# Performance work log

Hardware: AMD Instinct MI355X
Metric: run time of the kernel (lower is better)

The kernel has to match this reference:

```python
import jax, jax.numpy as jnp
import numpy as np

SIG = [1, 1, 1, 1, -1]  # Cl(4,1)
NVEC = 5
GA = 1 << NVEC  # 32


def _build_gp_table():
    # Cayley table for the geometric product on blades indexed by bitmask.
    G = np.zeros((GA, GA, GA), np.float32)
    for a in range(GA):
        for b in range(GA):
            s = 0
            t = a >> 1
            while t:
                s += bin(t & b).count('1')
                t >>= 1
            sign = -1.0 if (s & 1) else 1.0
            common = a & b
            for i in range(NVEC):
                if (common >> i) & 1:
                    sign *= SIG[i]
            G[a, b, a ^ b] = sign
    return G

GP_TABLE = jnp.asarray(_build_gp_table())


def geometric_product(x, y):
    return jnp.einsum('...i,...j,ijk->...k', x, y, GP_TABLE)


def manifold_norm(x):
    # normalize each multivector onto the unit sphere in R^32
    return x / (jnp.linalg.norm(x, axis=-1, keepdims=True) + 1e-6)


def versor_linear(x, W, b):
    # channel mixing shared across multivector components: x [..., in, ga]
    return jnp.einsum('...ig,oi->...og', x, W) + b


def layer_norm2d(x, w, b):
    # LayerNorm over last two dims [D, ga] jointly
    mu = jnp.mean(x, axis=(-2, -1), keepdims=True)
    var = jnp.var(x, axis=(-2, -1), keepdims=True)
    return (x - mu) / jnp.sqrt(var + 1e-5) * w + b


def attention(x, Wq, bq, Wk, bk, Wv, bv, Wo, bo, n_heads):
    B, S, D, G = x.shape
    dh = D // n_heads
    q = versor_linear(x, Wq, bq).reshape(B, S, n_heads, dh, G)
    k = versor_linear(x, Wk, bk).reshape(B, S, n_heads, dh, G)
    v = versor_linear(x, Wv, bv).reshape(B, S, n_heads, dh, G)
    scale = 1.0 / np.sqrt(dh * G).astype(np.float32)
    scores = jnp.einsum('bshdg,bthdg->bhst', q, k) * scale
    probs = jax.nn.softmax(scores, axis=-1)
    o = jnp.einsum('bhst,bthdg->bshdg', probs, v).reshape(B, S, D, G)
    return versor_linear(o, Wo, bo)


N_HEADS = 8


def forward(x, Wq, bq, Wk, bk, Wv, bv, Wo, bo, ln1_w, ln1_b, ln2_w, ln2_b,
            gamma1, gamma2, W1, b1, W2, b2, Wr, br, Wc, bc):
    L = Wq.shape[0]
    for l in range(L):
        h = attention(layer_norm2d(x, ln1_w[l], ln1_b[l]),
                      Wq[l], bq[l], Wk[l], bk[l], Wv[l], bv[l], Wo[l], bo[l], N_HEADS)
        x = manifold_norm(x + gamma1[l] * h)
        m = versor_linear(layer_norm2d(x, ln2_w[l], ln2_b[l]), W1[l], b1[l])
        m = versor_linear(jnp.tanh(m), W2[l], b2[l])
        x = manifold_norm(x + gamma2[l] * m)
    # RecursiveRotorAccumulator: log(S)-step inclusive scan of rotors
    delta = versor_linear(x, Wr, br)
    rot = 0.5 * delta
    rot = rot.at[..., 0].add(1.0)
    rot = manifold_norm(rot)
    S = x.shape[1]
    step = 1
    while step < S:
        left = rot[:, :-step]
        right = rot[:, step:]
        comb = manifold_norm(geometric_product(right, left))
        rot = jnp.concatenate([rot[:, :step], comb], axis=1)
        step *= 2
    pooled = rot[:, -1]  # [B, D, ga]
    logits = pooled.reshape(pooled.shape[0], -1) @ Wc.T + bc
    return logits


def setup_inputs() -> dict:
    key = jax.random.key(0)
    B, S, D, G, L, NC = 8, 256, 64, GA, 4, 1000
    E = 4 * D  # expansion hidden
    ks = jax.random.split(key, 16)
    sd = 0.02
    inp = {
        'x': jax.random.normal(ks[0], (B, S, D, G), jnp.float32),
        'Wq': jax.random.normal(ks[1], (L, D, D), jnp.float32) * sd,
        'bq': jnp.zeros((L, D, G), jnp.float32),
        'Wk': jax.random.normal(ks[2], (L, D, D), jnp.float32) * sd,
        'bk': jnp.zeros((L, D, G), jnp.float32),
        'Wv': jax.random.normal(ks[3], (L, D, D), jnp.float32) * sd,
        'bv': jnp.zeros((L, D, G), jnp.float32),
        'Wo': jax.random.normal(ks[4], (L, D, D), jnp.float32) * sd,
        'bo': jnp.zeros((L, D, G), jnp.float32),
        'ln1_w': jnp.ones((L, D, G), jnp.float32),
        'ln1_b': jnp.zeros((L, D, G), jnp.float32),
        'ln2_w': jnp.ones((L, D, G), jnp.float32),
        'ln2_b': jnp.zeros((L, D, G), jnp.float32),
        'gamma1': 1e-5 * jnp.ones((L, D, G), jnp.float32),
        'gamma2': 1e-5 * jnp.ones((L, D, G), jnp.float32),
        'W1': jax.random.normal(ks[5], (L, E, D), jnp.float32) * sd,
        'b1': jnp.zeros((L, E, G), jnp.float32),
        'W2': jax.random.normal(ks[6], (L, D, E), jnp.float32) * sd,
        'b2': jnp.zeros((L, D, G), jnp.float32),
        'Wr': jax.random.normal(ks[7], (D, D), jnp.float32) * sd,
        'br': jnp.zeros((D, G), jnp.float32),
        'Wc': jax.random.normal(ks[8], (NC, D * G), jnp.float32) * sd,
        'bc': jnp.zeros((NC,), jnp.float32),
    }
    return inp


def reference(x, Wq, bq, Wk, bk, Wv, bv, Wo, bo, ln1_w, ln1_b, ln2_w, ln2_b,
              gamma1, gamma2, W1, b1, W2, b2, Wr, br, Wc, bc):
    return forward(x, Wq, bq, Wk, bk, Wv, bv, Wo, bo, ln1_w, ln1_b, ln2_w, ln2_b,
                   gamma1, gamma2, W1, b1, W2, b2, Wr, br, Wc, bc)
```

## Files before the change

kernel.cpp:

```cpp
#include <hip/hip_runtime.h>
#include <hip/hip_bf16.h>

constexpr int kB  = 8;
constexpr int kS  = 256;
constexpr int kD  = 64;
constexpr int kG  = 32;
constexpr int kE  = 256;
constexpr int kNH = 8;
constexpr int kHD = 256;
constexpr int kDG = kD * kG;
constexpr int kT  = kB * kS;
constexpr int kNC = 1000;

using bf16x8 = __attribute__((ext_vector_type(8))) short;
using f32x4  = __attribute__((ext_vector_type(4))) float;

__device__ __forceinline__ short f2bf(float f) {
    unsigned u = __float_as_uint(f);
    unsigned r = (u + 0x7FFFu + ((u >> 16) & 1u)) >> 16;
    return (short)r;
}

__device__ __forceinline__ float tanh_fast(float x) {
    float a = fabsf(x);
    float e = __expf(-2.f * a);
    float d = 1.f + e;
    float r = __builtin_amdgcn_rcpf(d);
    r = r * (2.f - d * r);
    float t = (1.f - e) * r;
    return copysignf(t, x);
}

__global__ __launch_bounds__(256) void cvtw_kernel(
    const float* __restrict__ Wq, const float* __restrict__ Wk,
    const float* __restrict__ Wv, const float* __restrict__ Wo,
    const float* __restrict__ W1, const float* __restrict__ W2,
    unsigned short* __restrict__ dst) {
    int idx = (blockIdx.x * 256 + threadIdx.x) * 4;
    const float* src; int off;
    if      (idx <  16384) { src = Wq; off = 0; }
    else if (idx <  32768) { src = Wk; off = 16384; }
    else if (idx <  49152) { src = Wv; off = 32768; }
    else if (idx <  65536) { src = Wo; off = 49152; }
    else if (idx < 131072) { src = W1; off = 65536; }
    else                   { src = W2; off = 131072; }
    const float4 v = *(const float4*)(src + (idx - off));
    *(short4*)&dst[idx] = make_short4(f2bf(v.x), f2bf(v.y), f2bf(v.z), f2bf(v.w));
}

__global__ __launch_bounds__(256) void prep_tr_kernel(
    const float* __restrict__ bq, const float* __restrict__ bk,
    const float* __restrict__ bv, const float* __restrict__ bo,
    const float* __restrict__ b2, const float* __restrict__ gm1,
    const float* __restrict__ gm2, const float* __restrict__ ln2w,
    const float* __restrict__ ln2b, const float* __restrict__ ln1w,
    const float* __restrict__ ln1b, const float* __restrict__ b1,
    float* __restrict__ dst) {
    __shared__ float lt[32 * 257];
    const int a = blockIdx.x >> 2, l = blockIdx.x & 3;
    const float* srcs[12] = {bq, bk, bv, bo, b2, gm1, gm2, ln2w, ln2b, ln1w, ln1b, b1};
    const int R  = (a == 11) ? 256 : 64;
    const int sh = (a == 11) ? 8 : 6;
    const float* src = srcs[a] + (size_t)l * R * 32;
    float* out = dst + a * 8192 + l * R * 32;
    const int tid = threadIdx.x;
    for (int j = tid; j < R * 32; j += 256) lt[(j & 31) * (R + 1) + (j >> 5)] = src[j];
    __syncthreads();
    for (int k = tid; k < R * 32; k += 256) {
        int g = k >> sh, r = k & (R - 1);
        out[k] = lt[g * (R + 1) + r];
    }
}

__global__ __launch_bounds__(256) void ln_kernel(const float* __restrict__ Xin,
                                                 const float* __restrict__ w,
                                                 const float* __restrict__ b,
                                                 unsigned short* __restrict__ A,
                                                 float* __restrict__ XT) {
    int t = blockIdx.x, tid = threadIdx.x;
    const float* xp = Xin + (size_t)t * kDG;
    __shared__ float r1[256], r2[256];
    __shared__ short st[32 * 72];
    __shared__ float xf[32 * 68];
    float v[8], s = 0.f, ss = 0.f;
#pragma unroll
    for (int j = 0; j < 8; j++) {
        float x = xp[tid + j * 256];
        v[j] = x; s += x; ss += x * x;
        int jj = tid + j * 256;
        xf[(jj & 31) * 68 + (jj >> 5)] = x;
    }
    r1[tid] = s; r2[tid] = ss; __syncthreads();
    for (int o = 128; o > 0; o >>= 1) {
        if (tid < o) { r1[tid] += r1[tid + o]; r2[tid] += r2[tid + o]; }
        __syncthreads();
    }
    float mean = r1[0] * (1.f / kDG);
    float var  = r2[0] * (1.f / kDG) - mean * mean;
    float rstd = rsqrtf(var + 1e-5f);
#pragma unroll
    for (int j = 0; j < 8; j++) {
        int jj = tid + j * 256;
        float val = (v[j] - mean) * rstd * w[jj] + b[jj];
        st[(jj & 31) * 72 + (jj >> 5)] = f2bf(val);
    }
    __syncthreads();
    bf16x8 ov = *(const bf16x8*)&st[(tid >> 3) * 72 + (tid & 7) * 8];
    *(bf16x8*)&A[(size_t)t * kDG + tid * 8] = ov;
    const int row = tid >> 3, col = (tid & 7) * 8;
    float* xo = XT + (size_t)t * kDG + tid * 8;
    *(float4*)(xo + 0) = *(const float4*)&xf[row * 68 + col + 0];
    *(float4*)(xo + 4) = *(const float4*)&xf[row * 68 + col + 4];
}

__global__ __launch_bounds__(256) void vlinT_kernel(const float* __restrict__ XT,
                                                    const float* __restrict__ W,
                                                    const float* __restrict__ bias,
                                                    float* __restrict__ OutT) {
    __shared__ float sx[32 * 65];
    __shared__ float sw[kD * kD];
    int t = blockIdx.x, tid = threadIdx.x;
    const float* xp = XT + (size_t)t * kDG;
    for (int j = tid; j < kDG; j += 256) sx[(j >> 6) * 65 + (j & 63)] = xp[j];
    for (int j = tid; j < kD * kD; j += 256) sw[j] = W[j];
    __syncthreads();
    int g = tid & 31, ob = tid >> 5;
    int b = t >> 8, s = t & 255;
    float* op = OutT + ((size_t)b * kD * kS + s) * kG;
    for (int o = ob; o < kD; o += 8) {
        float acc = bias[o * kG + g];
        const float* wr = sw + o * kD;
#pragma unroll
        for (int i = 0; i < kD; i++) acc += wr[i] * sx[g * 65 + i];
        op[(size_t)o * kS * kG + g] = acc;
    }
}

template<bool LAST>
__global__ __launch_bounds__(128, 4) void mega_kernel(
    const unsigned short* __restrict__ O,
    const unsigned short* __restrict__ Woh, const float* __restrict__ boT,
    const float* __restrict__ gm1T,
    const float* __restrict__ ln2wT, const float* __restrict__ ln2bT,
    const unsigned short* __restrict__ W1h, const float* __restrict__ b1T,
    const unsigned short* __restrict__ W2h, const float* __restrict__ b2T,
    const float* __restrict__ gm2T,
    const float* __restrict__ ln1wT, const float* __restrict__ ln1bT,
    float* __restrict__ XT,
    const unsigned short* __restrict__ Wqh, const unsigned short* __restrict__ Wkh,
    const unsigned short* __restrict__ Wvh,
    const float* __restrict__ bqT, const float* __restrict__ bkT,
    const float* __restrict__ bvT,
    unsigned short* __restrict__ Q, unsigned short* __restrict__ K,
    unsigned short* __restrict__ V) {
    constexpr int AS = 72;
    constexpr int MS = 264;
    __shared__ short sA[32 * AS];
    __shared__ short sM[32 * MS];
    __shared__ float sred[4];

    const int tid = threadIdx.x;
    const int w = tid >> 6, lane = tid & 63;
    const int l16 = lane & 15, quad = lane >> 4;
    const int tok = blockIdx.x;
    const size_t tb = (size_t)tok * kDG;

    float xv[2][2][4];
    {
        const unsigned short* xp = O + tb;
        bf16x8 bfr[2][2];
#pragma unroll
        for (int c = 0; c < 2; ++c)
#pragma unroll
            for (int nt = 0; nt < 2; ++nt)
                bfr[c][nt] = *(const bf16x8*)&xp[(nt * 16 + l16) * kD + c * 32 + quad * 8];

        f32x4 accW[2][2];
#pragma unroll
        for (int mt = 0; mt < 2; ++mt)
#pragma unroll
            for (int nt = 0; nt < 2; ++nt) accW[mt][nt] = (f32x4){0.f, 0.f, 0.f, 0.f};
#pragma unroll
        for (int mt = 0; mt < 2; ++mt)
#pragma unroll
            for (int c = 0; c < 2; ++c) {
                bf16x8 afr = *(const bf16x8*)&Woh[(w * 32 + mt * 16 + l16) * kD + c * 32 + quad * 8];
#pragma unroll
                for (int nt = 0; nt < 2; ++nt)
                    accW[mt][nt] = __builtin_amdgcn_mfma_f32_16x16x32_bf16(afr, bfr[c][nt], accW[mt][nt], 0, 0, 0);
            }

        float s = 0.f, ss = 0.f;
#pragma unroll
        for (int mt = 0; mt < 2; ++mt) {
            int o0 = w * 32 + mt * 16 + quad * 4;
            float vv[2][4];
#pragma unroll
            for (int nt = 0; nt < 2; ++nt) {
                int g = nt * 16 + l16;
                const float4 b4 = *(const float4*)&boT[g * kD + o0];
                const float4 g4 = *(const float4*)&gm1T[g * kD + o0];
                const float4 xi = *(const float4*)&XT[tb + g * kD + o0];
#pragma unroll
                for (int r = 0; r < 4; ++r)
                    vv[nt][r] = (&xi.x)[r] + (&g4.x)[r] * (accW[mt][nt][r] + (&b4.x)[r]);
            }
#pragma unroll
            for (int r = 0; r < 4; ++r) {
                float sq = vv[0][r] * vv[0][r] + vv[1][r] * vv[1][r];
#pragma unroll
                for (int off = 1; off < 16; off <<= 1) sq += __shfl_xor(sq, off, 64);
                float rn = 1.f / (sqrtf(sq) + 1e-6f);
#pragma unroll
                for (int nt = 0; nt < 2; ++nt) {
                    float x = vv[nt][r] * rn;
                    xv[mt][nt][r] = x;
                    s += x; ss = fmaf(x, x, ss);
                }
            }
        }
#pragma unroll
        for (int off = 1; off < 64; off <<= 1) {
            s += __shfl_xor(s, off, 64); ss += __shfl_xor(ss, off, 64);
        }
        if (lane == 0) { sred[w] = s; sred[2 + w] = ss; }
        __syncthreads();
        float st = sred[0] + sred[1], sst = sred[2] + sred[3];
        float mean = st * (1.f / kDG);
        float var  = sst * (1.f / kDG) - mean * mean;
        float rstd = rsqrtf(var + 1e-5f);
#pragma unroll
        for (int mt = 0; mt < 2; ++mt)
#pragma unroll
            for (int nt = 0; nt < 2; ++nt) {
                int g = nt * 16 + l16;
                int o0 = w * 32 + mt * 16 + quad * 4;
                const float4 w4 = *(const float4*)&ln2wT[g * kD + o0];
                const float4 b4 = *(const float4*)&ln2bT[g * kD + o0];
                short4 s4;
#pragma unroll
                for (int r = 0; r < 4; ++r)
                    (&s4.x)[r] = f2bf((xv[mt][nt][r] - mean) * rstd * (&w4.x)[r] + (&b4.x)[r]);
                *(short4*)&sA[g * AS + o0] = s4;
            }
    }
    __syncthreads();

    {
        bf16x8 afrA[2][2];
#pragma unroll
        for (int c = 0; c < 2; ++c)
#pragma unroll
            for (int nt = 0; nt < 2; ++nt)
                afrA[c][nt] = *(const bf16x8*)&sA[(nt * 16 + l16) * AS + c * 32 + quad * 8];

        f32x4 acc1[8][2];
#pragma unroll
        for (int mt = 0; mt < 8; ++mt)
#pragma unroll
            for (int nt = 0; nt < 2; ++nt) acc1[mt][nt] = (f32x4){0.f, 0.f, 0.f, 0.f};
#pragma unroll
        for (int mt = 0; mt < 8; ++mt)
#pragma unroll
            for (int c = 0; c < 2; ++c) {
                bf16x8 afr = *(const bf16x8*)&W1h[((w * 8 + mt) * 16 + l16) * kD + c * 32 + quad * 8];
#pragma unroll
                for (int nt = 0; nt < 2; ++nt)
                    acc1[mt][nt] = __builtin_amdgcn_mfma_f32_16x16x32_bf16(afr, afrA[c][nt], acc1[mt][nt], 0, 0, 0);
            }
#pragma unroll
        for (int mt = 0; mt < 8; ++mt)
#pragma unroll
            for (int nt = 0; nt < 2; ++nt) {
                int g = nt * 16 + l16;
                int e0 = (w * 8 + mt) * 16 + quad * 4;
                const float4 b4 = *(const float4*)&b1T[g * kE + e0];
                short4 s4;
#pragma unroll
                for (int r = 0; r < 4; ++r)
                    (&s4.x)[r] = f2bf(tanh_fast(acc1[mt][nt][r] + (&b4.x)[r]));
                *(short4*)&sM[g * MS + e0] = s4;
            }
    }
    __syncthreads();

    f32x4 acc2[2][2];
#pragma unroll
    for (int mt = 0; mt < 2; ++mt)
#pragma unroll
        for (int nt = 0; nt < 2; ++nt) acc2[mt][nt] = (f32x4){0.f, 0.f, 0.f, 0.f};
#pragma unroll
    for (int c = 0; c < 8; ++c) {
        bf16x8 bq[2];
#pragma unroll
        for (int nt = 0; nt < 2; ++nt)
            bq[nt] = *(const bf16x8*)&sM[(nt * 16 + l16) * MS + c * 32 + quad * 8];
#pragma unroll
        for (int mt = 0; mt < 2; ++mt) {
            bf16x8 afr = *(const bf16x8*)&W2h[(w * 32 + mt * 16 + l16) * kE + c * 32 + quad * 8];
#pragma unroll
            for (int nt = 0; nt < 2; ++nt)
                acc2[mt][nt] = __builtin_amdgcn_mfma_f32_16x16x32_bf16(afr, bq[nt], acc2[mt][nt], 0, 0, 0);
        }
    }

    float yv[2][2][4];
    float s2 = 0.f, ss2 = 0.f;
#pragma unroll
    for (int mt = 0; mt < 2; ++mt) {
        int o0 = w * 32 + mt * 16 + quad * 4;
        float vv[2][4];
#pragma unroll
        for (int nt = 0; nt < 2; ++nt) {
            int g = nt * 16 + l16;
            const float4 b4 = *(const float4*)&b2T[g * kD + o0];
            const float4 g4 = *(const float4*)&gm2T[g * kD + o0];
#pragma unroll
            for (int r = 0; r < 4; ++r)
                vv[nt][r] = xv[mt][nt][r] + (&g4.x)[r] * (acc2[mt][nt][r] + (&b4.x)[r]);
        }
#pragma unroll
        for (int r = 0; r < 4; ++r) {
            float sq = vv[0][r] * vv[0][r] + vv[1][r] * vv[1][r];
#pragma unroll
            for (int off = 1; off < 16; off <<= 1) sq += __shfl_xor(sq, off, 64);
            float rn = 1.f / (sqrtf(sq) + 1e-6f);
#pragma unroll
            for (int nt = 0; nt < 2; ++nt) {
                float x = vv[nt][r] * rn;
                yv[mt][nt][r] = x;
                s2 += x; ss2 = fmaf(x, x, ss2);
            }
        }
#pragma unroll
        for (int nt = 0; nt < 2; ++nt) {
            int g = nt * 16 + l16;
            float4 xo;
#pragma unroll
            for (int r = 0; r < 4; ++r) (&xo.x)[r] = yv[mt][nt][r];
            *(float4*)&XT[tb + g * kD + o0] = xo;
        }
    }
    if constexpr (LAST) return;

#pragma unroll
    for (int off = 1; off < 64; off <<= 1) {
        s2 += __shfl_xor(s2, off, 64); ss2 += __shfl_xor(ss2, off, 64);
    }
    if (lane == 0) { sred[w] = s2; sred[2 + w] = ss2; }
    __syncthreads();
    {
        float st = sred[0] + sred[1], sst = sred[2] + sred[3];
        float mean = st * (1.f / kDG);
        float var  = sst * (1.f / kDG) - mean * mean;
        float rstd = rsqrtf(var + 1e-5f);
#pragma unroll
        for (int mt = 0; mt < 2; ++mt)
#pragma unroll
            for (int nt = 0; nt < 2; ++nt) {
                int g = nt * 16 + l16;
                int o0 = w * 32 + mt * 16 + quad * 4;
                const float4 w4 = *(const float4*)&ln1wT[g * kD + o0];
                const float4 b4 = *(const float4*)&ln1bT[g * kD + o0];
                short4 s4;
#pragma unroll
                for (int r = 0; r < 4; ++r)
                    (&s4.x)[r] = f2bf((yv[mt][nt][r] - mean) * rstd * (&w4.x)[r] + (&b4.x)[r]);
                *(short4*)&sA[g * AS + o0] = s4;
            }
    }
    __syncthreads();

    {
        bf16x8 afrA[2][2];
#pragma unroll
        for (int c = 0; c < 2; ++c)
#pragma unroll
            for (int nt = 0; nt < 2; ++nt)
                afrA[c][nt] = *(const bf16x8*)&sA[(nt * 16 + l16) * AS + c * 32 + quad * 8];

        const unsigned short* Wp[3] = {Wqh, Wkh, Wvh};
        const float* Bp[3] = {bqT, bkT, bvT};
        unsigned short* Op[3] = {Q, K, V};
#pragma unroll
        for (int m = 0; m < 3; ++m) {
            f32x4 acc3[2][2];
#pragma unroll
            for (int mt = 0; mt < 2; ++mt)
#pragma unroll
                for (int nt = 0; nt < 2; ++nt) acc3[mt][nt] = (f32x4){0.f, 0.f, 0.f, 0.f};
#pragma unroll
            for (int mt = 0; mt < 2; ++mt)
#pragma unroll
                for (int c = 0; c < 2; ++c) {
                    bf16x8 afr = *(const bf16x8*)&Wp[m][(w * 32 + mt * 16 + l16) * kD + c * 32 + quad * 8];
#pragma unroll
                    for (int nt = 0; nt < 2; ++nt)
                        acc3[mt][nt] = __builtin_amdgcn_mfma_f32_16x16x32_bf16(afr, afrA[c][nt], acc3[mt][nt], 0, 0, 0);
                }
            unsigned short* op = Op[m] + tb;
#pragma unroll
            for (int mt = 0; mt < 2; ++mt)
#pragma unroll
                for (int nt = 0; nt < 2; ++nt) {
                    int g = nt * 16 + l16;
                    int o0 = w * 32 + mt * 16 + quad * 4;
                    const float4 b4 = *(const float4*)&Bp[m][g * kD + o0];
#pragma unroll
                    for (int r = 0; r < 4; ++r)
                        op[(o0 + r) * kG + g] = (unsigned short)f2bf(acc3[mt][nt][r] + (&b4.x)[r]);
                }
        }
    }
}

__global__ __launch_bounds__(256, 3) void gemm_qkv_kernel(
    const unsigned short* __restrict__ X,
    const unsigned short* __restrict__ Wqh, const unsigned short* __restrict__ Wkh,
    const unsigned short* __restrict__ Wvh,
    const float* __restrict__ bqT, const float* __restrict__ bkT, const float* __restrict__ bvT,
    unsigned short* __restrict__ Q, unsigned short* __restrict__ K, unsigned short* __restrict__ V) {
    constexpr int WS = 64 + 8;
    __shared__ short sW[3 * 64 * WS];

    const int tid = threadIdx.x, wave = tid >> 6, lane = tid & 63;
    const int l16 = lane & 15, quad = lane >> 4;
    const int tok = blockIdx.x * 4 + wave;

    const unsigned short* Wp[3] = {Wqh, Wkh, Wvh};
#pragma unroll
    for (int w = 0; w < 3; ++w)
        for (int j = tid * 8; j < 64 * 64; j += 2048) {
            int o = j >> 6, i = j & 63;
            *(bf16x8*)&sW[w * 64 * WS + o * WS + i] = *(const bf16x8*)(Wp[w] + j);
        }

    const unsigned short* xp = X + (size_t)tok * kDG;
    bf16x8 bfr[2][2];
#pragma unroll
    for (int c = 0; c < 2; ++c)
#pragma unroll
        for (int nt = 0; nt < 2; ++nt)
            bfr[c][nt] = *(const bf16x8*)&xp[(nt * 16 + l16) * kD + c * 32 + quad * 8];
    __syncthreads();

    f32x4 acc[3][4][2];
#pragma unroll
    for (int w = 0; w < 3; ++w)
#pragma unroll
        for (int mt = 0; mt < 4; ++mt)
#pragma unroll
            for (int nt = 0; nt < 2; ++nt) acc[w][mt][nt] = (f32x4){0.f, 0.f, 0.f, 0.f};

#pragma unroll
    for (int w = 0; w < 3; ++w)
#pragma unroll
        for (int mt = 0; mt < 4; ++mt)
#pragma unroll
            for (int c = 0; c < 2; ++c) {
                bf16x8 afr = *(const bf16x8*)&sW[w * 64 * WS + (mt * 16 + l16) * WS + c * 32 + quad * 8];
#pragma unroll
                for (int nt = 0; nt < 2; ++nt)
                    acc[w][mt][nt] = __builtin_amdgcn_mfma_f32_16x16x32_bf16(afr, bfr[c][nt], acc[w][mt][nt], 0, 0, 0);
            }

    unsigned short* Op[3] = {Q, K, V};
    const float* Bp[3] = {bqT, bkT, bvT};
#pragma unroll
    for (int w = 0; w < 3; ++w) {
        unsigned short* op = Op[w] + (size_t)tok * kDG;
#pragma unroll
        for (int mt = 0; mt < 4; ++mt)
#pragma unroll
            for (int nt = 0; nt < 2; ++nt) {
                int g = nt * 16 + l16;
                int o0 = mt * 16 + quad * 4;
                const float4 b4 = *(const float4*)&Bp[w][g * kD + o0];
#pragma unroll
                for (int r = 0; r < 4; ++r)
                    op[(o0 + r) * kG + g] = (unsigned short)f2bf(acc[w][mt][nt][r] + (&b4.x)[r]);
            }
    }
}

constexpr int QSTR = 264;
constexpr int VSTR = 40;

__global__ __launch_bounds__(256) void attn_mfma_kernel(const unsigned short* __restrict__ Q,
                                                        const unsigned short* __restrict__ K,
                                                        const unsigned short* __restrict__ V,
                                                        unsigned short* __restrict__ O) {
    __shared__ short sQ[64 * QSTR];
    __shared__ short sKV[2][256 * VSTR];

    const int qt = blockIdx.x, h = blockIdx.y, b = blockIdx.z;
    const int tid = threadIdx.x;
    const int wave = tid >> 6, lane = tid & 63;
    const int l16 = lane & 15, quad = lane >> 4;

    const size_t bh = (size_t)b * kS * kDG + (size_t)h * kHD;

#pragma unroll
    for (int it = 0; it < 8; ++it) {
        int j = it * 2048 + tid * 8;
        int row = j >> 8, col = j & 255;
        *(bf16x8*)&sQ[row * QSTR + col] =
            *(const bf16x8*)(Q + bh + (size_t)(qt * 64 + row) * kDG + col);
    }
#pragma unroll
    for (int it = 0; it < 4; ++it) {
        int j = it * 2048 + tid * 8;
        int row = j >> 8, col = j & 255;
        *(bf16x8*)&sKV[0][row * QSTR + col] =
            *(const bf16x8*)(K + bh + (size_t)row * kDG + col);
    }
    __syncthreads();

    bf16x8 afrag[8];
    {
        int row = wave * 16 + l16;
#pragma unroll
        for (int c = 0; c < 8; ++c)
            afrag[c] = *(const bf16x8*)&sQ[row * QSTR + c * 32 + quad * 8];
    }

    f32x4 acc[16];
#pragma unroll
    for (int i = 0; i < 16; ++i) acc[i] = (f32x4){0.f, 0.f, 0.f, 0.f};

    for (int kt = 0; kt < 8; ++kt) {
        bf16x8 kpre[4];
        if (kt < 7) {
#pragma unroll
            for (int it = 0; it < 4; ++it) {
                int j = it * 2048 + tid * 8;
                int row = j >> 8, col = j & 255;
                kpre[it] = *(const bf16x8*)(K + bh + (size_t)((kt + 1) * 32 + row) * kDG + col);
            }
        }
        const short* kb = sKV[kt & 1];
#pragma unroll
        for (int nt = 0; nt < 2; ++nt) {
            int key = nt * 16 + l16;
            f32x4 a = acc[kt * 2 + nt];
#pragma unroll
            for (int c = 0; c < 8; ++c) {
                bf16x8 bfrag = *(const bf16x8*)&kb[key * QSTR + c * 32 + quad * 8];
                a = __builtin_amdgcn_mfma_f32_16x16x32_bf16(afrag[c], bfrag, a, 0, 0, 0);
            }
            acc[kt * 2 + nt] = a;
        }
        if (kt < 7) {
            short* nb = sKV[(kt + 1) & 1];
#pragma unroll
            for (int it = 0; it < 4; ++it) {
                int j = it * 2048 + tid * 8;
                int row = j >> 8, col = j & 255;
                *(bf16x8*)&nb[row * QSTR + col] = kpre[it];
            }
            __syncthreads();
        }
    }

    float inv[4];
#pragma unroll
    for (int r = 0; r < 4; ++r) {
        float m = -1e30f;
#pragma unroll
        for (int t = 0; t < 16; ++t) m = fmaxf(m, acc[t][r]);
#pragma unroll
        for (int off = 1; off < 16; off <<= 1) m = fmaxf(m, __shfl_xor(m, off, 16));
        float s = 0.f;
#pragma unroll
        for (int t = 0; t < 16; ++t) {
            float p = __expf((acc[t][r] - m) * 0.0625f);
            acc[t][r] = p; s += p;
        }
#pragma unroll
        for (int off = 1; off < 16; off <<= 1) s += __shfl_xor(s, off, 16);
        inv[r] = 1.f / s;
    }

#pragma unroll
    for (int t = 0; t < 16; ++t)
#pragma unroll
        for (int r = 0; r < 4; ++r)
            sQ[(wave * 16 + quad * 4 + r) * QSTR + t * 16 + l16] = f2bf(acc[t][r]);

    {
        int kb = tid >> 5;
#pragma unroll
        for (int it = 0; it < 2; ++it) {
            int db = (tid & 31) + it * 32;
            short4 vr[4];
#pragma unroll
            for (int r = 0; r < 4; ++r)
                vr[r] = *(const short4*)(V + bh + (size_t)(kb * 4 + r) * kDG + db * 4);
#pragma unroll
            for (int i = 0; i < 4; ++i) {
                short4 p = make_short4((&vr[0].x)[i], (&vr[1].x)[i],
                                       (&vr[2].x)[i], (&vr[3].x)[i]);
                *(short4*)&sKV[0][(db * 4 + i) * VSTR + kb * 4] = p;
            }
        }
    }
    __syncthreads();

    f32x4 oacc[16];
#pragma unroll
    for (int i = 0; i < 16; ++i) oacc[i] = (f32x4){0.f, 0.f, 0.f, 0.f};

    for (int vt = 0; vt < 8; ++vt) {
        short4 vpre[8];
        if (vt < 7) {
            int kb = tid >> 5;
#pragma unroll
            for (int it = 0; it < 2; ++it) {
                int db = (tid & 31) + it * 32;
#pragma unroll
                for (int r = 0; r < 4; ++r)
                    vpre[it * 4 + r] = *(const short4*)(V + bh + (size_t)((vt + 1) * 32 + kb * 4 + r) * kDG + db * 4);
            }
        }
        const short* vb = sKV[vt & 1];
        bf16x8 pfrag = *(const bf16x8*)&sQ[(wave * 16 + l16) * QSTR + vt * 32 + quad * 8];
#pragma unroll
        for (int dt = 0; dt < 16; ++dt) {
            bf16x8 vfrag = *(const bf16x8*)&vb[(dt * 16 + l16) * VSTR + quad * 8];
            oacc[dt] = __builtin_amdgcn_mfma_f32_16x16x32_bf16(pfrag, vfrag, oacc[dt], 0, 0, 0);
        }
        if (vt < 7) {
            short* nb = sKV[(vt + 1) & 1];
            int kb = tid >> 5;
#pragma unroll
            for (int it = 0; it < 2; ++it) {
                int db = (tid & 31) + it * 32;
#pragma unroll
                for (int i = 0; i < 4; ++i) {
                    short4 p = make_short4((&vpre[it * 4 + 0].x)[i], (&vpre[it * 4 + 1].x)[i],
                                           (&vpre[it * 4 + 2].x)[i], (&vpre[it * 4 + 3].x)[i]);
                    *(short4*)&nb[(db * 4 + i) * VSTR + kb * 4] = p;
                }
            }
            __syncthreads();
        }
    }

    {
        const size_t ob = (size_t)(b * kS + qt * 64 + wave * 16 + quad * 4) * kDG + h * 8;
#pragma unroll
        for (int gg = 0; gg < 2; ++gg) {
            int g = gg * 16 + l16;
#pragma unroll
            for (int r = 0; r < 4; ++r) {
                bf16x8 pk;
#pragma unroll
                for (int k = 0; k < 8; ++k)
                    pk[k] = f2bf(oacc[k * 2 + gg][r] * inv[r]);
                *(bf16x8*)&O[ob + (size_t)r * kDG + g * kD] = pk;
            }
        }
    }
}

constexpr int pc_ce(unsigned v) { int c = 0; while (v) { c += v & 1; v >>= 1; } return c; }
constexpr unsigned gp_mask_ce(int a) {
    unsigned m = 0;
    for (int c = 0; c < 32; ++c) {
        int b = a ^ c;
        int s = (a & b) >> 4;
        for (int t = a >> 1; t; t >>= 1) s += pc_ce(t & b);
        if (s & 1) m |= (1u << c);
    }
    return m;
}

template<int A>
__device__ __forceinline__ void gp_term(const float* x, const float* y, float* acc) {
    constexpr unsigned m = gp_mask_ce(A);
    const float xa = x[A], nxa = -xa;
#pragma unroll
    for (int c = 0; c < 32; ++c)
        acc[c] = fmaf(((m >> c) & 1u) ? nxa : xa, y[A ^ c], acc[c]);
}

__device__ __forceinline__ void gp_mn_t(const float* x, const float* y, float* out) {
    float acc[32];
#pragma unroll
    for (int c = 0; c < 32; ++c) acc[c] = 0.f;
    gp_term<0>(x, y, acc);  gp_term<1>(x, y, acc);  gp_term<2>(x, y, acc);  gp_term<3>(x, y, acc);
    gp_term<4>(x, y, acc);  gp_term<5>(x, y, acc);  gp_term<6>(x, y, acc);  gp_term<7>(x, y, acc);
    gp_term<8>(x, y, acc);  gp_term<9>(x, y, acc);  gp_term<10>(x, y, acc); gp_term<11>(x, y, acc);
    gp_term<12>(x, y, acc); gp_term<13>(x, y, acc); gp_term<14>(x, y, acc); gp_term<15>(x, y, acc);
    gp_term<16>(x, y, acc); gp_term<17>(x, y, acc); gp_term<18>(x, y, acc); gp_term<19>(x, y, acc);
    gp_term<20>(x, y, acc); gp_term<21>(x, y, acc); gp_term<22>(x, y, acc); gp_term<23>(x, y, acc);
    gp_term<24>(x, y, acc); gp_term<25>(x, y, acc); gp_term<26>(x, y, acc); gp_term<27>(x, y, acc);
    gp_term<28>(x, y, acc); gp_term<29>(x, y, acc); gp_term<30>(x, y, acc); gp_term<31>(x, y, acc);
    float ss = 0.f;
#pragma unroll
    for (int c = 0; c < 32; ++c) ss = fmaf(acc[c], acc[c], ss);
    float r = 1.f / (sqrtf(ss) + 1e-6f);
#pragma unroll
    for (int c = 0; c < 32; ++c) out[c] = acc[c] * r;
}

__device__ __forceinline__ void leaf_load(const float* base, float* v) {
#pragma unroll
    for (int i = 0; i < 8; ++i) {
        const float4 f = *(const float4*)(base + i * 4);
        v[i * 4 + 0] = 0.5f * f.x; v[i * 4 + 1] = 0.5f * f.y;
        v[i * 4 + 2] = 0.5f * f.z; v[i * 4 + 3] = 0.5f * f.w;
    }
    v[0] += 1.f;
    float ss = 0.f;
#pragma unroll
    for (int c = 0; c < 32; ++c) ss = fmaf(v[c], v[c], ss);
    float r = 1.f / (sqrtf(ss) + 1e-6f);
#pragma unroll
    for (int c = 0; c < 32; ++c) v[c] *= r;
}

__global__ __launch_bounds__(256) void scanreg_kernel(const float* __restrict__ DT,
                                                      float* __restrict__ pooled) {
    const int wave = threadIdx.x >> 6, lane = threadIdx.x & 63;
    const int seq = blockIdx.x * 4 + wave;
    const float* base = DT + ((size_t)seq * kS + lane * 4) * kG;

    float R[32], Y[32], P[32], Xa[32], Yb[32];

    leaf_load(base, R);
    for (int j = 1; j < 4; ++j) {
        leaf_load(base + j * kG, Y);
        gp_mn_t(Y, R, R);
    }

    for (int step = 1; step < 64; step <<= 1) {
        const bool up = lane & step;
#pragma unroll
        for (int c = 0; c < 32; ++c) P[c] = __shfl_xor(R[c], step, 64);
#pragma unroll
        for (int c = 0; c < 32; ++c) {
            Xa[c] = up ? R[c] : P[c];
            Yb[c] = up ? P[c] : R[c];
        }
        gp_mn_t(Xa, Yb, R);
    }

    if (lane == 0) {
        float* op = pooled + (size_t)seq * kG;
#pragma unroll
        for (int i = 0; i < 8; ++i)
            *(float4*)(op + i * 4) = make_float4(R[i * 4], R[i * 4 + 1], R[i * 4 + 2], R[i * 4 + 3]);
    }
}

__global__ __launch_bounds__(256) void cls2_kernel(const float* __restrict__ P,
                                                   const float* __restrict__ Wc,
                                                   const float* __restrict__ bc,
                                                   float* __restrict__ out) {
    __shared__ float sp[kB * kDG];
    const int tid = threadIdx.x, wave = tid >> 6, lane = tid & 63;
    for (int j = tid * 4; j < kB * kDG; j += 1024)
        *(float4*)&sp[j] = *(const float4*)(P + j);
    __syncthreads();

    const int c = blockIdx.x * 4 + wave;
    const float* w = Wc + (size_t)c * kDG;
    float acc[kB];
#pragma unroll
    for (int b = 0; b < kB; ++b) acc[b] = 0.f;
#pragma unroll
    for (int cc = 0; cc < 8; ++cc) {
        const float4 w4 = *(const float4*)(w + cc * 256 + lane * 4);
#pragma unroll
        for (int b = 0; b < kB; ++b) {
            const float4 p4 = *(const float4*)&sp[b * kDG + cc * 256 + lane * 4];
            acc[b] += w4.x * p4.x + w4.y * p4.y + w4.z * p4.z + w4.w * p4.w;
        }
    }
#pragma unroll
    for (int b = 0; b < kB; ++b)
#pragma unroll
        for (int off = 32; off > 0; off >>= 1) acc[b] += __shfl_xor(acc[b], off, 64);
    if (lane == 0) {
        float bias = bc[c];
#pragma unroll
        for (int b = 0; b < kB; ++b) out[b * kNC + c] = acc[b] + bias;
    }
}

extern "C" void kernel_launch(void* const* d_in, const int* in_sizes, int n_in,
                              void* d_out, int out_size, void* d_ws, size_t ws_size,
                              hipStream_t stream) {
    const float* x_in = (const float*)d_in[0];
    const float* Wq   = (const float*)d_in[1];
    const float* bq   = (const float*)d_in[2];
    const float* Wk   = (const float*)d_in[3];
    const float* bk   = (const float*)d_in[4];
    const float* Wv   = (const float*)d_in[5];
    const float* bv   = (const float*)d_in[6];
    const float* Wo   = (const float*)d_in[7];
    const float* bo   = (const float*)d_in[8];
    const float* ln1w = (const float*)d_in[9];
    const float* ln1b = (const float*)d_in[10];
    const float* ln2w = (const float*)d_in[11];
    const float* ln2b = (const float*)d_in[12];
    const float* gm1  = (const float*)d_in[13];
    const float* gm2  = (const float*)d_in[14];
    const float* W1   = (const float*)d_in[15];
    const float* b1   = (const float*)d_in[16];
    const float* W2   = (const float*)d_in[17];
    const float* b2   = (const float*)d_in[18];
    const float* Wr   = (const float*)d_in[19];
    const float* br   = (const float*)d_in[20];
    const float* Wc   = (const float*)d_in[21];
    const float* bc   = (const float*)d_in[22];

    const size_t NEL = (size_t)kT * kDG;
    float* F  = (float*)d_ws;
    float* XT = F;
    unsigned short* Abf = (unsigned short*)(F + NEL);
    unsigned short* Qh = (unsigned short*)(F + 2 * NEL);
    unsigned short* Kh = (unsigned short*)(F + 3 * NEL);
    unsigned short* Vh = (unsigned short*)(F + 4 * NEL);
    unsigned short* Wb = (unsigned short*)(F + 5 * NEL);
    float* PT = F + 3 * NEL + NEL / 2;
    float* pooled = F + 2 * NEL;
    float* DT = F + NEL;

    cvtw_kernel<<<192, 256, 0, stream>>>(Wq, Wk, Wv, Wo, W1, W2, Wb);
    prep_tr_kernel<<<48, 256, 0, stream>>>(bq, bk, bv, bo, b2, gm1, gm2,
                                           ln2w, ln2b, ln1w, ln1b, b1, PT);
    unsigned short* Wqh = Wb;
    unsigned short* Wkh = Wb + 16384;
    unsigned short* Wvh = Wb + 32768;
    unsigned short* Woh = Wb + 49152;
    unsigned short* W1h = Wb + 65536;
    unsigned short* W2h = Wb + 131072;

    auto bqT   = [&](int l) { return PT + 0     + l * 2048; };
    auto bkT   = [&](int l) { return PT + 8192  + l * 2048; };
    auto bvT   = [&](int l) { return PT + 16384 + l * 2048; };
    auto boT   = [&](int l) { return PT + 24576 + l * 2048; };
    auto b2T   = [&](int l) { return PT + 32768 + l * 2048; };
    auto gm1T  = [&](int l) { return PT + 40960 + l * 2048; };
    auto gm2T  = [&](int l) { return PT + 49152 + l * 2048; };
    auto ln2wT = [&](int l) { return PT + 57344 + l * 2048; };
    auto ln2bT = [&](int l) { return PT + 65536 + l * 2048; };
    auto ln1wT = [&](int l) { return PT + 73728 + l * 2048; };
    auto ln1bT = [&](int l) { return PT + 81920 + l * 2048; };
    auto b1T   = [&](int l) { return PT + 90112 + l * 8192; };

    ln_kernel<<<kT, 256, 0, stream>>>(x_in, ln1w, ln1b, Abf, XT);
    gemm_qkv_kernel<<<kT / 4, 256, 0, stream>>>(Abf,
        Wqh, Wkh, Wvh, bqT(0), bkT(0), bvT(0), Qh, Kh, Vh);

    for (int l = 0; l < 4; l++) {
        attn_mfma_kernel<<<dim3(4, kNH, kB), 256, 0, stream>>>(Qh, Kh, Vh, Abf);
        if (l < 3)
            mega_kernel<false><<<kT, 128, 0, stream>>>(Abf,
                Woh + l * 4096, boT(l), gm1T(l), ln2wT(l), ln2bT(l),
                W1h + l * 16384, b1T(l), W2h + l * 16384, b2T(l), gm2T(l),
                ln1wT(l + 1), ln1bT(l + 1), XT,
                Wqh + (l + 1) * 4096, Wkh + (l + 1) * 4096, Wvh + (l + 1) * 4096,
                bqT(l + 1), bkT(l + 1), bvT(l + 1), Qh, Kh, Vh);
        else
            mega_kernel<true><<<kT, 128, 0, stream>>>(Abf,
                Woh + l * 4096, boT(l), gm1T(l), ln2wT(l), ln2bT(l),
                W1h + l * 16384, b1T(l), W2h + l * 16384, b2T(l), gm2T(l),
                nullptr, nullptr, XT,
                nullptr, nullptr, nullptr, nullptr, nullptr, nullptr,
                nullptr, nullptr, nullptr);
    }

    vlinT_kernel<<<kT, 256, 0, stream>>>(XT, Wr, br, DT);
    scanreg_kernel<<<kB * kD / 4, 256, 0, stream>>>(DT, pooled);
    cls2_kernel<<<kNC / 4, 256, 0, stream>>>(pooled, Wc, bc, (float*)d_out);
}
```

Measured before the change: 521.1 us.

## Prefetch MLP/QKV weight fragments early and halve attention query tile

```diff
diff --git a/kernel.cpp b/kernel.cpp
--- a/kernel.cpp
+++ b/kernel.cpp
@@ -137,7 +137,7 @@
 }
 
 template<bool LAST>
-__global__ __launch_bounds__(128, 4) void mega_kernel(
+__global__ __launch_bounds__(128, 3) void mega_kernel(
     const unsigned short* __restrict__ O,
     const unsigned short* __restrict__ Woh, const float* __restrict__ boT,
     const float* __restrict__ gm1T,
@@ -166,6 +166,7 @@
     const size_t tb = (size_t)tok * kDG;
 
     float xv[2][2][4];
+    bf16x8 w1f[8];
     {
         const unsigned short* xp = O + tb;
         bf16x8 bfr[2][2];
@@ -189,6 +190,12 @@
                 for (int nt = 0; nt < 2; ++nt)
                     accW[mt][nt] = __builtin_amdgcn_mfma_f32_16x16x32_bf16(afr, bfr[c][nt], accW[mt][nt], 0, 0, 0);
             }
+
+#pragma unroll
+        for (int mt = 0; mt < 4; ++mt)
+#pragma unroll
+            for (int c = 0; c < 2; ++c)
+                w1f[mt * 2 + c] = *(const bf16x8*)&W1h[((w * 8 + mt) * 16 + l16) * kD + c * 32 + quad * 8];
 
         float s = 0.f, ss = 0.f;
 #pragma unroll
@@ -246,6 +253,7 @@
     }
     __syncthreads();
 
+    bf16x8 w2f[16];
     {
         bf16x8 afrA[2][2];
 #pragma unroll
@@ -254,22 +262,28 @@
             for (int nt = 0; nt < 2; ++nt)
                 afrA[c][nt] = *(const bf16x8*)&sA[(nt * 16 + l16) * AS + c * 32 + quad * 8];
 
-        f32x4 acc1[8][2];
-#pragma unroll
-        for (int mt = 0; mt < 8; ++mt)
+        f32x4 acc1[4][2];
+#pragma unroll
+        for (int mt = 0; mt < 4; ++mt)
 #pragma unroll
             for (int nt = 0; nt < 2; ++nt) acc1[mt][nt] = (f32x4){0.f, 0.f, 0.f, 0.f};
 #pragma unroll
-        for (int mt = 0; mt < 8; ++mt)
-#pragma unroll
-            for (int c = 0; c < 2; ++c) {
-                bf16x8 afr = *(const bf16x8*)&W1h[((w * 8 + mt) * 16 + l16) * kD + c * 32 + quad * 8];
+        for (int mt = 0; mt < 4; ++mt)
+#pragma unroll
+            for (int c = 0; c < 2; ++c)
 #pragma unroll
                 for (int nt = 0; nt < 2; ++nt)
-                    acc1[mt][nt] = __builtin_amdgcn_mfma_f32_16x16x32_bf16(afr, afrA[c][nt], acc1[mt][nt], 0, 0, 0);
-            }
-#pragma unroll
-        for (int mt = 0; mt < 8; ++mt)
+                    acc1[mt][nt] = __builtin_amdgcn_mfma_f32_16x16x32_bf16(w1f[mt * 2 + c], afrA[c][nt], acc1[mt][nt], 0, 0, 0);
+
+        bf16x8 w1g[8];
+#pragma unroll
+        for (int mt = 0; mt < 4; ++mt)
+#pragma unroll
+            for (int c = 0; c < 2; ++c)
+                w1g[mt * 2 + c] = *(const bf16x8*)&W1h[((w * 8 + 4 + mt) * 16 + l16) * kD + c * 32 + quad * 8];
+
+#pragma unroll
+        for (int mt = 0; mt < 4; ++mt)
 #pragma unroll
             for (int nt = 0; nt < 2; ++nt) {
                 int g = nt * 16 + l16;
@@ -281,6 +295,39 @@
                     (&s4.x)[r] = f2bf(tanh_fast(acc1[mt][nt][r] + (&b4.x)[r]));
                 *(short4*)&sM[g * MS + e0] = s4;
             }
+
+        f32x4 acc1b[4][2];
+#pragma unroll
+        for (int mt = 0; mt < 4; ++mt)
+#pragma unroll
+            for (int nt = 0; nt < 2; ++nt) acc1b[mt][nt] = (f32x4){0.f, 0.f, 0.f, 0.f};
+#pragma unroll
+        for (int mt = 0; mt < 4; ++mt)
+#pragma unroll
+            for (int c = 0; c < 2; ++c)
+#pragma unroll
+                for (int nt = 0; nt < 2; ++nt)
+                    acc1b[mt][nt] = __builtin_amdgcn_mfma_f32_16x16x32_bf16(w1g[mt * 2 + c], afrA[c][nt], acc1b[mt][nt], 0, 0, 0);
+
+#pragma unroll
+        for (int mt = 0; mt < 2; ++mt)
+#pragma unroll
+            for (int c = 0; c < 8; ++c)
+                w2f[mt * 8 + c] = *(const bf16x8*)&W2h[(w * 32 + mt * 16 + l16) * kE + c * 32 + quad * 8];
+
+#pragma unroll
+        for (int mt = 0; mt < 4; ++mt)
+#pragma unroll
+            for (int nt = 0; nt < 2; ++nt) {
+                int g = nt * 16 + l16;
+                int e0 = (w * 8 + 4 + mt) * 16 + quad * 4;
+                const float4 b4 = *(const float4*)&b1T[g * kE + e0];
+                short4 s4;
+#pragma unroll
+                for (int r = 0; r < 4; ++r)
+                    (&s4.x)[r] = f2bf(tanh_fast(acc1b[mt][nt][r] + (&b4.x)[r]));
+                *(short4*)&sM[g * MS + e0] = s4;
+            }
     }
     __syncthreads();
 
@@ -296,12 +343,22 @@
         for (int nt = 0; nt < 2; ++nt)
             bq[nt] = *(const bf16x8*)&sM[(nt * 16 + l16) * MS + c * 32 + quad * 8];
 #pragma unroll
-        for (int mt = 0; mt < 2; ++mt) {
-            bf16x8 afr = *(const bf16x8*)&W2h[(w * 32 + mt * 16 + l16) * kE + c * 32 + quad * 8];
+        for (int mt = 0; mt < 2; ++mt)
 #pragma unroll
             for (int nt = 0; nt < 2; ++nt)
-                acc2[mt][nt] = __builtin_amdgcn_mfma_f32_16x16x32_bf16(afr, bq[nt], acc2[mt][nt], 0, 0, 0);
-        }
+                acc2[mt][nt] = __builtin_amdgcn_mfma_f32_16x16x32_bf16(w2f[mt * 8 + c], bq[nt], acc2[mt][nt], 0, 0, 0);
+    }
+
+    bf16x8 wqf[12];
+    if constexpr (!LAST) {
+        const unsigned short* Wp[3] = {Wqh, Wkh, Wvh};
+#pragma unroll
+        for (int m = 0; m < 3; ++m)
+#pragma unroll
+            for (int mt = 0; mt < 2; ++mt)
+#pragma unroll
+                for (int c = 0; c < 2; ++c)
+                    wqf[m * 4 + mt * 2 + c] = *(const bf16x8*)&Wp[m][(w * 32 + mt * 16 + l16) * kD + c * 32 + quad * 8];
     }
 
     float yv[2][2][4];
@@ -379,7 +436,6 @@
             for (int nt = 0; nt < 2; ++nt)
                 afrA[c][nt] = *(const bf16x8*)&sA[(nt * 16 + l16) * AS + c * 32 + quad * 8];
 
-        const unsigned short* Wp[3] = {Wqh, Wkh, Wvh};
         const float* Bp[3] = {bqT, bkT, bvT};
         unsigned short* Op[3] = {Q, K, V};
 #pragma unroll
@@ -392,12 +448,10 @@
 #pragma unroll
             for (int mt = 0; mt < 2; ++mt)
 #pragma unroll
-                for (int c = 0; c < 2; ++c) {
-                    bf16x8 afr = *(const bf16x8*)&Wp[m][(w * 32 + mt * 16 + l16) * kD + c * 32 + quad * 8];
+                for (int c = 0; c < 2; ++c)
 #pragma unroll
                     for (int nt = 0; nt < 2; ++nt)
-                        acc3[mt][nt] = __builtin_amdgcn_mfma_f32_16x16x32_bf16(afr, afrA[c][nt], acc3[mt][nt], 0, 0, 0);
-                }
+                        acc3[mt][nt] = __builtin_amdgcn_mfma_f32_16x16x32_bf16(wqf[m * 4 + mt * 2 + c], afrA[c][nt], acc3[mt][nt], 0, 0, 0);
             unsigned short* op = Op[m] + tb;
 #pragma unroll
             for (int mt = 0; mt < 2; ++mt)
@@ -486,11 +540,11 @@
 constexpr int QSTR = 264;
 constexpr int VSTR = 40;
 
-__global__ __launch_bounds__(256) void attn_mfma_kernel(const unsigned short* __restrict__ Q,
+__global__ __launch_bounds__(128) void attn_mfma_kernel(const unsigned short* __restrict__ Q,
                                                         const unsigned short* __restrict__ K,
                                                         const unsigned short* __restrict__ V,
                                                         unsigned short* __restrict__ O) {
-    __shared__ short sQ[64 * QSTR];
+    __shared__ short sQ[32 * QSTR];
     __shared__ short sKV[2][256 * VSTR];
 
     const int qt = blockIdx.x, h = blockIdx.y, b = blockIdx.z;
@@ -502,14 +556,14 @@
 
 #pragma unroll
     for (int it = 0; it < 8; ++it) {
-        int j = it * 2048 + tid * 8;
+        int j = it * 1024 + tid * 8;
         int row = j >> 8, col = j & 255;
         *(bf16x8*)&sQ[row * QSTR + col] =
-            *(const bf16x8*)(Q + bh + (size_t)(qt * 64 + row) * kDG + col);
-    }
-#pragma unroll
-    for (int it = 0; it < 4; ++it) {
-        int j = it * 2048 + tid * 8;
+            *(const bf16x8*)(Q + bh + (size_t)(qt * 32 + row) * kDG + col);
+    }
+#pragma unroll
+    for (int it = 0; it < 8; ++it) {
+        int j = it * 1024 + tid * 8;
         int row = j >> 8, col = j & 255;
         *(bf16x8*)&sKV[0][row * QSTR + col] =
             *(const bf16x8*)(K + bh + (size_t)row * kDG + col);
@@ -529,11 +583,11 @@
     for (int i = 0; i < 16; ++i) acc[i] = (f32x4){0.f, 0.f, 0.f, 0.f};
 
     for (int kt = 0; kt < 8; ++kt) {
-        bf16x8 kpre[4];
+        bf16x8 kpre[8];
         if (kt < 7) {
 #pragma unroll
-            for (int it = 0; it < 4; ++it) {
-                int j = it * 2048 + tid * 8;
+            for (int it = 0; it < 8; ++it) {
+                int j = it * 1024 + tid * 8;
                 int row = j >> 8, col = j & 255;
                 kpre[it] = *(const bf16x8*)(K + bh + (size_t)((kt + 1) * 32 + row) * kDG + col);
             }
@@ -553,8 +607,8 @@
         if (kt < 7) {
             short* nb = sKV[(kt + 1) & 1];
 #pragma unroll
-            for (int it = 0; it < 4; ++it) {
-                int j = it * 2048 + tid * 8;
+            for (int it = 0; it < 8; ++it) {
+                int j = it * 1024 + tid * 8;
                 int row = j >> 8, col = j & 255;
                 *(bf16x8*)&nb[row * QSTR + col] = kpre[it];
             }
@@ -588,21 +642,19 @@
             sQ[(wave * 16 + quad * 4 + r) * QSTR + t * 16 + l16] = f2bf(acc[t][r]);
 
     {
-        int kb = tid >> 5;
-#pragma unroll
-        for (int it = 0; it < 2; ++it) {
-            int db = (tid & 31) + it * 32;
-            short4 vr[4];
-#pragma unroll
-            for (int r = 0; r < 4; ++r)
-                vr[r] = *(const short4*)(V + bh + (size_t)(kb * 4 + r) * kDG + db * 4);
-#pragma unroll
-            for (int i = 0; i < 4; ++i) {
-                short4 p = make_short4((&vr[0].x)[i], (&vr[1].x)[i],
-                                       (&vr[2].x)[i], (&vr[3].x)[i]);
-                *(short4*)&sKV[0][(db * 4 + i) * VSTR + kb * 4] = p;
-            }
-        }
+        const int db = tid & 63, kh = tid >> 6;
+        short4 vr[16];
+#pragma unroll
+        for (int r = 0; r < 16; ++r)
+            vr[r] = *(const short4*)(V + bh + (size_t)(kh * 16 + r) * kDG + db * 4);
+#pragma unroll
+        for (int i = 0; i < 4; ++i)
+#pragma unroll
+            for (int gq = 0; gq < 4; ++gq) {
+                short4 p = make_short4((&vr[gq * 4 + 0].x)[i], (&vr[gq * 4 + 1].x)[i],
+                                       (&vr[gq * 4 + 2].x)[i], (&vr[gq * 4 + 3].x)[i]);
+                *(short4*)&sKV[0][(db * 4 + i) * VSTR + kh * 16 + gq * 4] = p;
+            }
     }
     __syncthreads();
 
@@ -611,16 +663,12 @@
     for (int i = 0; i < 16; ++i) oacc[i] = (f32x4){0.f, 0.f, 0.f, 0.f};
 
     for (int vt = 0; vt < 8; ++vt) {
-        short4 vpre[8];
+        short4 vpre[16];
         if (vt < 7) {
-            int kb = tid >> 5;
-#pragma unroll
-            for (int it = 0; it < 2; ++it) {
-                int db = (tid & 31) + it * 32;
-#pragma unroll
-                for (int r = 0; r < 4; ++r)
-                    vpre[it * 4 + r] = *(const short4*)(V + bh + (size_t)((vt + 1) * 32 + kb * 4 + r) * kDG + db * 4);
-            }
+            const int db = tid & 63, kh = tid >> 6;
+#pragma unroll
+            for (int r = 0; r < 16; ++r)
+                vpre[r] = *(const short4*)(V + bh + (size_t)((vt + 1) * 32 + kh * 16 + r) * kDG + db * 4);
         }
         const short* vb = sKV[vt & 1];
         bf16x8 pfrag = *(const bf16x8*)&sQ[(wave * 16 + l16) * QSTR + vt * 32 + quad * 8];
@@ -630,24 +678,22 @@
             oacc[dt] = __builtin_amdgcn_mfma_f32_16x16x32_bf16(pfrag, vfrag, oacc[dt], 0, 0, 0);
         }
         if (vt < 7) {
+            const int db = tid & 63, kh = tid >> 6;
             short* nb = sKV[(vt + 1) & 1];
-            int kb = tid >> 5;
-#pragma unroll
-            for (int it = 0; it < 2; ++it) {
-                int db = (tid & 31) + it * 32;
-#pragma unroll
-                for (int i = 0; i < 4; ++i) {
-                    short4 p = make_short4((&vpre[it * 4 + 0].x)[i], (&vpre[it * 4 + 1].x)[i],
-                                           (&vpre[it * 4 + 2].x)[i], (&vpre[it * 4 + 3].x)[i]);
-                    *(short4*)&nb[(db * 4 + i) * VSTR + kb * 4] = p;
+#pragma unroll
+            for (int i = 0; i < 4; ++i)
+#pragma unroll
+                for (int gq = 0; gq < 4; ++gq) {
+                    short4 p = make_short4((&vpre[gq * 4 + 0].x)[i], (&vpre[gq * 4 + 1].x)[i],
+                                           (&vpre[gq * 4 + 2].x)[i], (&vpre[gq * 4 + 3].x)[i]);
+                    *(short4*)&nb[(db * 4 + i) * VSTR + kh * 16 + gq * 4] = p;
                 }
-            }
             __syncthreads();
         }
     }
 
     {
-        const size_t ob = (size_t)(b * kS + qt * 64 + wave * 16 + quad * 4) * kDG + h * 8;
+        const size_t ob = (size_t)(b * kS + qt * 32 + wave * 16 + quad * 4) * kDG + h * 8;
 #pragma unroll
         for (int gg = 0; gg < 2; ++gg) {
             int g = gg * 16 + l16;
@@ -856,7 +902,7 @@
         Wqh, Wkh, Wvh, bqT(0), bkT(0), bvT(0), Qh, Kh, Vh);
 
     for (int l = 0; l < 4; l++) {
-        attn_mfma_kernel<<<dim3(4, kNH, kB), 256, 0, stream>>>(Qh, Kh, Vh, Abf);
+        attn_mfma_kernel<<<dim3(8, kNH, kB), 128, 0, stream>>>(Qh, Kh, Vh, Abf);
         if (l < 3)
             mega_kernel<false><<<kT, 128, 0, stream>>>(Abf,
                 Woh + l * 4096, boT(l), gm1T(l), ln2wT(l), ln2bT(l),
```

Result: no change. 530.2 us (+1.8%).
